# Performance work log

Hardware: AMD Instinct MI355X
Metric: run time of the kernel (lower is better)

## Reference

```python
import jax, jax.numpy as jnp
import numpy as np

BATCH = 4
N1 = 131072   # stage-1 voxels (total over batch)
N2 = 32768    # stage-2 (stride-2 downsampled) voxels
D_MODEL = 128
D_INNER = 2 * D_MODEL
D_STATE = 16
D_CONV = 4
DT_RANK = 8   # ceil(d_model / 16)
EPS = 1e-5


def _ln(x, g, b):
    mu = x.mean(-1, keepdims=True)
    v = ((x - mu) ** 2).mean(-1, keepdims=True)
    return (x - mu) * jax.lax.rsqrt(v + EPS) * g + b


def _causal_conv(x, w, b):
    # x: [B,L,Di], w: [Di,K] -> depthwise causal conv1d
    y = jax.lax.conv_general_dilated(
        x.transpose(0, 2, 1), w[:, None, :], (1,), [(D_CONV - 1, 0)],
        dimension_numbers=('NCH', 'OIH', 'NCH'), feature_group_count=D_INNER)
    return y.transpose(0, 2, 1) + b


def _mamba_block(x, ln_g, ln_b, in_w, conv_w, conv_b, xproj_w, dtproj_w, dtproj_b, A_log, Dp, out_w):
    # create_block: LayerNorm -> Mamba mixer (selective scan); returns hidden states
    h = _ln(x, ln_g, ln_b)
    xz = h @ in_w.T                          # [B,L,2*Di]
    xc, z = jnp.split(xz, 2, axis=-1)
    xc = jax.nn.silu(_causal_conv(xc, conv_w, conv_b))
    dbl = xc @ xproj_w.T                     # [B,L,dt_rank+2*d_state]
    dt = jax.nn.softplus(dbl[..., :DT_RANK] @ dtproj_w.T + dtproj_b)  # [B,L,Di]
    Bm = dbl[..., DT_RANK:DT_RANK + D_STATE]
    Cm = dbl[..., DT_RANK + D_STATE:]
    A = -jnp.exp(A_log)                      # [Di,ds]

    def step(hst, inp):
        dt_t, b_t, c_t, u_t = inp            # [B,Di],[B,ds],[B,ds],[B,Di]
        hst = jnp.exp(dt_t[..., None] * A) * hst + (dt_t * u_t)[..., None] * b_t[:, None, :]
        return hst, jnp.einsum('bds,bs->bd', hst, c_t)

    h0 = jnp.zeros((x.shape[0], D_INNER, D_STATE), x.dtype)
    xs = (dt.transpose(1, 0, 2), Bm.transpose(1, 0, 2), Cm.transpose(1, 0, 2), xc.transpose(1, 0, 2))
    _, ys = jax.lax.scan(step, h0, xs)       # ys: [L,B,Di]
    y = ys.transpose(1, 0, 2) + xc * Dp
    y = y * jax.nn.silu(z)
    return y @ out_w.T


def _mamba_params(key):
    ks = jax.random.split(key, 6)
    s = lambda k, sh, sc: jax.random.normal(k, sh, jnp.float32) * sc
    return dict(
        ln_g=jnp.ones((D_MODEL,), jnp.float32), ln_b=jnp.zeros((D_MODEL,), jnp.float32),
        in_w=s(ks[0], (2 * D_INNER, D_MODEL), 0.05),
        conv_w=s(ks[1], (D_INNER, D_CONV), 0.2), conv_b=jnp.zeros((D_INNER,), jnp.float32),
        xproj_w=s(ks[2], (DT_RANK + 2 * D_STATE, D_INNER), 0.05),
        dtproj_w=s(ks[3], (D_INNER, DT_RANK), 0.1), dtproj_b=s(ks[4], (D_INNER,), 0.1),
        A_log=jnp.log(jnp.tile(jnp.arange(1, D_STATE + 1, dtype=jnp.float32), (D_INNER, 1))),
        D=jnp.ones((D_INNER,), jnp.float32),
        out_w=s(ks[5], (D_MODEL, D_INNER), 0.05))


def setup_inputs():
    key = jax.random.key(0)
    k = jax.random.split(key, 10)
    inp = {
        'feats_s1': jax.random.normal(k[0], (N1, D_MODEL), jnp.float32),
        'feats_s2': jax.random.normal(k[1], (N2, D_MODEL), jnp.float32),
        'pos_s1': jax.random.uniform(k[2], (N1, 3), jnp.float32),
        'pos_s2': jax.random.uniform(k[3], (N2, 3), jnp.float32),
        'hilbert_s1': jax.random.randint(k[4], (N1,), 0, 1 << 30, jnp.int32),
        'hilbert_s2': jax.random.randint(k[5], (N2,), 0, 1 << 30, jnp.int32),
        'pe_w': jax.random.normal(k[6], (D_MODEL, 3), jnp.float32) * 0.1,
        'pe_b': jnp.zeros((D_MODEL,), jnp.float32),
        'norm_g': jnp.ones((D_MODEL,), jnp.float32), 'norm_b': jnp.zeros((D_MODEL,), jnp.float32),
        'normb_g': jnp.ones((D_MODEL,), jnp.float32), 'normb_b': jnp.zeros((D_MODEL,), jnp.float32),
    }
    for pref, kk in (('m1_', k[7]), ('m2_', k[8])):
        for n, v in _mamba_params(kk).items():
            inp[pref + n] = v
    return inp


def _forward(feats_s1, feats_s2, pos_s1, pos_s2, pe_w, pe_b, norm_g, norm_b, normb_g, normb_b,
             m1_ln_g, m1_ln_b, m1_in_w, m1_conv_w, m1_conv_b, m1_xproj_w, m1_dtproj_w, m1_dtproj_b, m1_A_log, m1_D, m1_out_w,
             m2_ln_g, m2_ln_b, m2_in_w, m2_conv_w, m2_conv_b, m2_xproj_w, m2_dtproj_w, m2_dtproj_b, m2_A_log, m2_D, m2_out_w,
             hilbert_s1, hilbert_s2):
    L1, L2 = N1 // BATCH, N2 // BATCH
    m1 = (m1_ln_g, m1_ln_b, m1_in_w, m1_conv_w, m1_conv_b, m1_xproj_w, m1_dtproj_w, m1_dtproj_b, m1_A_log, m1_D, m1_out_w)
    m2 = (m2_ln_g, m2_ln_b, m2_in_w, m2_conv_w, m2_conv_b, m2_xproj_w, m2_dtproj_w, m2_dtproj_b, m2_A_log, m2_D, m2_out_w)

    # stage 2: hilbert-order forward scan through mamba_layer1
    f2 = (feats_s2 + pos_s2 @ pe_w.T + pe_b).reshape(BATCH, L2, D_MODEL)
    o2 = jnp.argsort(hilbert_s2.reshape(BATCH, L2), axis=-1)          # inds_curt_to_next
    seq2 = jnp.take_along_axis(f2, o2[..., None], axis=1)
    out2 = _mamba_block(seq2, *m1)
    back2 = jnp.take_along_axis(out2, jnp.argsort(o2, axis=-1)[..., None], axis=1).reshape(N2, D_MODEL)
    out_s2 = _ln(back2, norm_g, norm_b)

    # stage 1: flipped hilbert-order (backward) scan through mamba_layer2
    f1 = (feats_s1 + pos_s1 @ pe_w.T + pe_b).reshape(BATCH, L1, D_MODEL)
    o1 = jnp.argsort(hilbert_s1.reshape(BATCH, L1), axis=-1)
    seq1 = jnp.take_along_axis(f1, o1[..., None], axis=1)[:, ::-1, :]
    out1 = _mamba_block(seq1, *m2)[:, ::-1, :]
    back1 = jnp.take_along_axis(out1, jnp.argsort(o1, axis=-1)[..., None], axis=1).reshape(N1, D_MODEL)
    out_s1 = _ln(back1, normb_g, normb_b)

    return jnp.concatenate([out_s1, out_s2], axis=0)   # [N1+N2, d_model]


def reference(feats_s1, feats_s2, pos_s1, pos_s2, pe_w, pe_b, norm_g, norm_b, normb_g, normb_b,
              m1_ln_g, m1_ln_b, m1_in_w, m1_conv_w, m1_conv_b, m1_xproj_w, m1_dtproj_w, m1_dtproj_b, m1_A_log, m1_D, m1_out_w,
              m2_ln_g, m2_ln_b, m2_in_w, m2_conv_w, m2_conv_b, m2_xproj_w, m2_dtproj_w, m2_dtproj_b, m2_A_log, m2_D, m2_out_w,
              hilbert_s1, hilbert_s2):
    return _forward(feats_s1, feats_s2, pos_s1, pos_s2, pe_w, pe_b, norm_g, norm_b, normb_g, normb_b,
                    m1_ln_g, m1_ln_b, m1_in_w, m1_conv_w, m1_conv_b, m1_xproj_w, m1_dtproj_w, m1_dtproj_b, m1_A_log, m1_D, m1_out_w,
                    m2_ln_g, m2_ln_b, m2_in_w, m2_conv_w, m2_conv_b, m2_xproj_w, m2_dtproj_w, m2_dtproj_b, m2_A_log, m2_D, m2_out_w,
                    hilbert_s1, hilbert_s2)
```

## Files before the change

### kernel.cpp

```cpp
#include <hip/hip_runtime.h>
#include <hip/hip_bf16.h>

#define DEV __device__ __forceinline__

constexpr int BATCH_ = 4;
constexpr int N1_ = 131072;
constexpr int N2_ = 32768;
constexpr int L1_ = N1_ / BATCH_;
constexpr int L2_ = N2_ / BATCH_;
constexpr int DM_ = 128;
constexpr int DI_ = 256;
constexpr int DS_ = 16;
constexpr int DTR_ = 8;
constexpr int TOT_ = N1_ + N2_;

constexpr int TA_ = 32;
constexpr int TAH_ = TA_ + 3;
constexpr int NTILE1_ = L1_ / TA_;
constexpr int NTILE2_ = L2_ / TA_;
constexpr int NTILES_ = 4 * NTILE1_ + 4 * NTILE2_;

constexpr int TS_ = 128;
constexpr int NCH1_ = L1_ / TS_;
constexpr int NCH2_ = L2_ / TS_;
constexpr int NCHUNKS_ = 4 * NCH1_ + 4 * NCH2_;

constexpr int NST_ = 160;

constexpr int IN1_OFF = 0;
constexpr int IN2_OFF = 65536;
constexpr int XP1_OFF = 131072;
constexpr int XP2_OFF = 143360;
constexpr int OW1_OFF = 155648;
constexpr int OW2_OFF = 188416;
constexpr int W16_TOT = 221184;

typedef short short8 __attribute__((ext_vector_type(8)));
typedef float f32x4 __attribute__((ext_vector_type(4)));

struct MP {
  const float* ln_g; const float* ln_b; const float* in_w;
  const float* conv_w; const float* conv_b; const float* xproj_w;
  const float* dtproj_w; const float* dtproj_b; const float* A_log;
  const float* Dp; const float* out_w;
};

DEV float softplusf(float x) {
  return fmaxf(x, 0.f) + __logf(1.f + __expf(-fabsf(x)));
}

DEV unsigned short f2bf(float f) {
  unsigned u = __builtin_bit_cast(unsigned, f);
  u += 0x7fffu + ((u >> 16) & 1u);
  return (unsigned short)(u >> 16);
}
DEV float bf2f(unsigned short s) {
  unsigned u = ((unsigned)s) << 16;
  return __builtin_bit_cast(float, u);
}

DEV void sort_tile_info(int tile, int& seg, int& tis, int& slotbase) {
  if (tile < 128) { seg = tile >> 5; tis = tile & 31; slotbase = seg * L1_; }
  else { seg = 4 + ((tile - 128) >> 3); tis = (tile - 128) & 7; slotbase = N1_ + (seg - 4) * L2_; }
}

__global__ __launch_bounds__(256) void k_prep(
    const float* __restrict__ in_w1, const float* __restrict__ xp1,
    const float* __restrict__ ow1,
    const float* __restrict__ in_w2, const float* __restrict__ xp2,
    const float* __restrict__ ow2,
    unsigned short* __restrict__ w16)
{
  const int i = blockIdx.x * 256 + threadIdx.x;
  if (i >= W16_TOT) return;
  float v;
  if (i < IN2_OFF) v = in_w1[i - IN1_OFF];
  else if (i < XP1_OFF) v = in_w2[i - IN2_OFF];
  else if (i < XP2_OFF) {
    const int j = i - XP1_OFF; const int r = j >> 8;
    v = (r < 40) ? xp1[j] : 0.f;
  } else if (i < OW1_OFF) {
    const int j = i - XP2_OFF; const int r = j >> 8;
    v = (r < 40) ? xp2[j] : 0.f;
  } else if (i < OW2_OFF) v = ow1[i - OW1_OFF];
  else v = ow2[i - OW2_OFF];
  w16[i] = f2bf(v);
}

__global__ __launch_bounds__(256) void k_hist(
    const int* __restrict__ hil1, const int* __restrict__ hil2,
    const unsigned* __restrict__ ksrc, unsigned* __restrict__ histg,
    int shift, int pass0)
{
  const int tile = blockIdx.x;
  int seg, tis, slotbase;
  sort_tile_info(tile, seg, tis, slotbase);
  const int tid = threadIdx.x;
  __shared__ unsigned h[1024];
  #pragma unroll
  for (int i = 0; i < 4; ++i) h[i * 256 + tid] = 0;
  __syncthreads();
  #pragma unroll
  for (int it = 0; it < 4; ++it) {
    const int li = tis * 1024 + it * 256 + tid;
    unsigned k;
    if (pass0) k = (unsigned)(seg < 4 ? hil1[seg * L1_ + li] : hil2[(seg - 4) * L2_ + li]);
    else       k = ksrc[slotbase + li];
    atomicAdd(&h[(k >> shift) & 1023u], 1u);
  }
  __syncthreads();
  #pragma unroll
  for (int i = 0; i < 4; ++i)
    histg[tile * 1024 + i * 256 + tid] = h[i * 256 + tid];
}

__global__ __launch_bounds__(256) void k_scanoff(
    const unsigned* __restrict__ histg, unsigned* __restrict__ offg)
{
  const int seg = blockIdx.x;
  const int ntiles = seg < 4 ? 32 : 8;
  const int tilebase = seg < 4 ? seg * 32 : 128 + (seg - 4) * 8;
  const int tid = threadIdx.x;
  const int d0 = tid * 4;
  unsigned tot[4] = {0, 0, 0, 0};
  for (int t = 0; t < ntiles; ++t) {
    const unsigned* hp = &histg[(size_t)(tilebase + t) * 1024 + d0];
    tot[0] += hp[0]; tot[1] += hp[1]; tot[2] += hp[2]; tot[3] += hp[3];
  }
  unsigned lp[4]; unsigned s = 0;
  #pragma unroll
  for (int j = 0; j < 4; ++j) { lp[j] = s; s += tot[j]; }
  const int lane = tid & 63, wv = tid >> 6;
  unsigned inc = s;
  #pragma unroll
  for (int off = 1; off < 64; off <<= 1) {
    unsigned v = (unsigned)__shfl_up((int)inc, off, 64);
    if (lane >= off) inc += v;
  }
  __shared__ unsigned wsum[4];
  if (lane == 63) wsum[wv] = inc;
  __syncthreads();
  unsigned wbase = 0;
  for (int w = 0; w < 4; ++w) if (w < wv) wbase += wsum[w];
  const unsigned base = wbase + inc - s;
  #pragma unroll
  for (int j = 0; j < 4; ++j) {
    unsigned run = base + lp[j];
    for (int t = 0; t < ntiles; ++t) {
      offg[(size_t)(tilebase + t) * 1024 + d0 + j] = run;
      run += histg[(size_t)(tilebase + t) * 1024 + d0 + j];
    }
  }
}

__global__ __launch_bounds__(256) void k_scatter(
    const int* __restrict__ hil1, const int* __restrict__ hil2,
    const unsigned* __restrict__ ksrc, const int* __restrict__ isrc,
    const unsigned* __restrict__ offg,
    unsigned* __restrict__ kdst, int* __restrict__ idst,
    int* __restrict__ o_all, int shift, int pass0, int last)
{
  const int tile = blockIdx.x;
  int seg, tis, slotbase;
  sort_tile_info(tile, seg, tis, slotbase);
  const int tid = threadIdx.x;
  const int lane = tid & 63, wv = tid >> 6;
  __shared__ unsigned runb[1024];
  __shared__ unsigned wcnt[4 * 1024];
  #pragma unroll
  for (int i = 0; i < 4; ++i) runb[i * 256 + tid] = offg[(size_t)tile * 1024 + i * 256 + tid];
  #pragma unroll
  for (int it = 0; it < 4; ++it) {
    #pragma unroll
    for (int i = 0; i < 16; ++i) wcnt[i * 256 + tid] = 0;
    __syncthreads();
    const int li = tis * 1024 + it * 256 + tid;
    unsigned k; int v;
    if (pass0) {
      k = (unsigned)(seg < 4 ? hil1[seg * L1_ + li] : hil2[(seg - 4) * L2_ + li]);
      v = li;
    } else {
      k = ksrc[slotbase + li]; v = isrc[slotbase + li];
    }
    const unsigned d = (k >> shift) & 1023u;
    unsigned long long m = ~0ull;
    #pragma unroll
    for (int b = 0; b < 10; ++b) {
      const unsigned long long bb = __ballot((int)((d >> b) & 1u));
      m &= ((d >> b) & 1u) ? bb : ~bb;
    }
    const unsigned lrank = (unsigned)__popcll(m & ((1ull << lane) - 1ull));
    wcnt[wv * 1024 + d] = (unsigned)__popcll(m);
    __syncthreads();
    unsigned prior = runb[d];
    for (int w = 0; w < 3; ++w) if (w < wv) prior += wcnt[w * 1024 + d];
    const unsigned pos = prior + lrank;
    if (last) o_all[slotbase + pos] = v;
    else { kdst[slotbase + pos] = k; idst[slotbase + pos] = v; }
    __syncthreads();
    #pragma unroll
    for (int i = 0; i < 4; ++i) {
      const int dd = i * 256 + tid;
      runb[dd] += wcnt[dd] + wcnt[1024 + dd] + wcnt[2048 + dd] + wcnt[3072 + dd];
    }
    __syncthreads();
  }
}

constexpr int HB_ = 136;
constexpr int XB_ = 264;
constexpr int OFF_HB16 = TAH_ * XB_ * 2;
constexpr int SMEM_A = OFF_HB16 + 48 * HB_ * 2;

__global__ __launch_bounds__(256) void k_phaseA(
    const float* __restrict__ feats1, const float* __restrict__ feats2,
    const float* __restrict__ pos1, const float* __restrict__ pos2,
    const float* __restrict__ pe_w, const float* __restrict__ pe_b,
    MP p1, MP p2, const int* __restrict__ o_all,
    const unsigned short* __restrict__ w16,
    __hip_bfloat16* __restrict__ xc_g, __hip_bfloat16* __restrict__ z_g,
    float* __restrict__ dbl_g)
{
  const int blk = blockIdx.x;
  bool is1; int b, tile;
  if (blk < 4 * NTILE1_) { is1 = true; b = blk / NTILE1_; tile = blk % NTILE1_; }
  else { const int r = blk - 4 * NTILE1_; is1 = false; b = r / NTILE2_; tile = r % NTILE2_; }
  const int L = is1 ? L1_ : L2_;
  const int slotbase = is1 ? b * L1_ : N1_ + b * L2_;
  const float* feats = is1 ? feats1 + (size_t)b * L1_ * DM_ : feats2 + (size_t)b * L2_ * DM_;
  const float* pos = is1 ? pos1 + (size_t)b * L1_ * 3 : pos2 + (size_t)b * L2_ * 3;
  const MP P = is1 ? p2 : p1;
  const unsigned short* iw16 = w16 + (is1 ? IN2_OFF : IN1_OFF);
  const unsigned short* xp16 = w16 + (is1 ? XP2_OFF : XP1_OFF);
  const bool rev = is1;
  const int t0 = tile * TA_;
  const int pstart = rev ? t0 : t0 - 3;
  const int lsh = rev ? 0 : 3;

  __shared__ char smem[SMEM_A];
  unsigned short* xcb16 = (unsigned short*)smem;
  unsigned short* hb16 = (unsigned short*)(smem + OFF_HB16);
  unsigned short* xc16 = xcb16;

  const int tid = threadIdx.x;
  const int lane = tid & 63, wv = tid >> 6;
  const int l15 = lane & 15, quad = lane >> 4;

  {
    unsigned* hz = (unsigned*)hb16;
    for (int i = tid; i < 13 * (HB_ / 2); i += 256)
      hz[TAH_ * (HB_ / 2) + i] = 0;
    const float pw00 = pe_w[lane * 3 + 0], pw01 = pe_w[lane * 3 + 1], pw02 = pe_w[lane * 3 + 2];
    const float pw10 = pe_w[(lane + 64) * 3 + 0], pw11 = pe_w[(lane + 64) * 3 + 1],
                pw12 = pe_w[(lane + 64) * 3 + 2];
    const float pb0 = pe_b[lane], pb1 = pe_b[lane + 64];
    const float g0 = P.ln_g[lane], g1 = P.ln_g[lane + 64];
    const float bt0 = P.ln_b[lane], bt1 = P.ln_b[lane + 64];
    #pragma unroll
    for (int k = 0; k < 9; ++k) {
      const int lt = wv + k * 4;
      if (lt >= TAH_) break;
      const int p = pstart + lt;
      unsigned short o0 = 0, o1 = 0;
      if (p >= 0 && p < L) {
        const int orig = o_all[slotbase + p];
        const float* fr = feats + (size_t)orig * DM_;
        const float* pr = pos + (size_t)orig * 3;
        const float c0 = pr[0], c1 = pr[1], c2 = pr[2];
        float x0 = fr[lane]      + c0 * pw00 + c1 * pw01 + c2 * pw02 + pb0;
        float x1 = fr[lane + 64] + c0 * pw10 + c1 * pw11 + c2 * pw12 + pb1;
        float s = x0 + x1, q = x0 * x0 + x1 * x1;
        #pragma unroll
        for (int off = 32; off; off >>= 1) {
          s += __shfl_xor(s, off, 64);
          q += __shfl_xor(q, off, 64);
        }
        const float mu = s * (1.f / 128.f);
        const float rs = rsqrtf(q * (1.f / 128.f) - mu * mu + 1e-5f);
        o0 = f2bf((x0 - mu) * rs * g0 + bt0);
        o1 = f2bf((x1 - mu) * rs * g1 + bt1);
      }
      hb16[lt * HB_ + lane]      = o0;
      hb16[lt * HB_ + lane + 64] = o1;
    }
  }
  __syncthreads();
  {
    short8 afr[3][4];
    #pragma unroll
    for (int mt = 0; mt < 3; ++mt)
      #pragma unroll
      for (int t = 0; t < 4; ++t)
        afr[mt][t] = *(const short8*)(hb16 + (mt * 16 + l15) * HB_ + t * 32 + quad * 8);
    for (int nn = 0; nn < 8; ++nn) {
      const int ntile = nn * 4 + wv;
      f32x4 acc[3];
      #pragma unroll
      for (int mt = 0; mt < 3; ++mt) acc[mt] = (f32x4){0.f, 0.f, 0.f, 0.f};
      #pragma unroll
      for (int t = 0; t < 4; ++t) {
        const short8 bfr = *(const short8*)(iw16 + (size_t)(ntile * 16 + l15) * DM_ + t * 32 + quad * 8);
        #pragma unroll
        for (int mt = 0; mt < 3; ++mt)
          acc[mt] = __builtin_amdgcn_mfma_f32_16x16x32_bf16(afr[mt][t], bfr, acc[mt], 0, 0, 0);
      }
      const int col = ntile * 16 + l15;
      if (col < 256) {
        #pragma unroll
        for (int mt = 0; mt < 3; ++mt)
          #pragma unroll
          for (int r = 0; r < 4; ++r) {
            const int row = mt * 16 + quad * 4 + r;
            if (row < TAH_) xcb16[row * XB_ + col] = f2bf(acc[mt][r]);
          }
      } else {
        #pragma unroll
        for (int mt = 0; mt < 3; ++mt)
          #pragma unroll
          for (int r = 0; r < 4; ++r) {
            const int row = mt * 16 + quad * 4 + r;
            const int m = row - lsh;
            if (m >= 0 && m < TA_)
              z_g[(size_t)(slotbase + t0 + m) * DI_ + (col - 256)] = __float2bfloat16(acc[mt][r]);
          }
      }
    }
  }
  __syncthreads();
  {
    const int d = tid;
    const float w0 = P.conv_w[d * 4 + 0], w1 = P.conv_w[d * 4 + 1],
                w2 = P.conv_w[d * 4 + 2], w3 = P.conv_w[d * 4 + 3];
    const float cb = P.conv_b[d];
    float x0 = bf2f(xcb16[0 * XB_ + d]), x1 = bf2f(xcb16[1 * XB_ + d]),
          x2 = bf2f(xcb16[2 * XB_ + d]);
    #pragma unroll
    for (int m = 0; m < TA_; ++m) {
      const float x3 = bf2f(xcb16[(m + 3) * XB_ + d]);
      float v;
      if (rev) v = w3 * x0 + w2 * x1 + w1 * x2 + w0 * x3;
      else     v = w0 * x0 + w1 * x1 + w2 * x2 + w3 * x3;
      v += cb;
      v = v * (1.f / (1.f + __expf(-v)));
      const unsigned short vb = f2bf(v);
      xc_g[(size_t)(slotbase + t0 + m) * DI_ + d] = __builtin_bit_cast(__hip_bfloat16, vb);
      xcb16[m * XB_ + d] = vb;
      x0 = x1; x1 = x2; x2 = x3;
    }
  }
  __syncthreads();
  if (wv < 3) {
    f32x4 acc0 = (f32x4){0.f,0.f,0.f,0.f}, acc1 = acc0;
    #pragma unroll
    for (int t = 0; t < 8; ++t) {
      const short8 bfr = *(const short8*)(xp16 + (size_t)(wv * 16 + l15) * DI_ + t * 32 + quad * 8);
      const short8 a0 = *(const short8*)(xc16 + (l15) * XB_ + t * 32 + quad * 8);
      const short8 a1 = *(const short8*)(xc16 + (16 + l15) * XB_ + t * 32 + quad * 8);
      acc0 = __builtin_amdgcn_mfma_f32_16x16x32_bf16(a0, bfr, acc0, 0, 0, 0);
      acc1 = __builtin_amdgcn_mfma_f32_16x16x32_bf16(a1, bfr, acc1, 0, 0, 0);
    }
    const int col = wv * 16 + l15;
    if (col < 40) {
      #pragma unroll
      for (int r = 0; r < 4; ++r) {
        dbl_g[(size_t)(slotbase + t0 + quad * 4 + r) * 40 + col] = acc0[r];
        dbl_g[(size_t)(slotbase + t0 + 16 + quad * 4 + r) * 40 + col] = acc1[r];
      }
    }
  }
}

struct ScanP {
  float Av[DS_]; float A0; bool fast;
  float dtw[DTR_]; float dtb;
};
DEV void load_scanp(const MP& P, int d, ScanP& sp) {
  #pragma unroll
  for (int s = 0; s < DS_; ++s) sp.Av[s] = -__expf(P.A_log[d * DS_ + s]);
  sp.A0 = sp.Av[0];
  bool f = true;
  #pragma unroll
  for (int s = 0; s < DS_; ++s)
    f = f && (fabsf(sp.Av[s] - (float)(s + 1) * sp.A0) <= 1e-3f * (float)(s + 1));
  sp.fast = f;
  #pragma unroll
  for (int r = 0; r < DTR_; ++r) sp.dtw[r] = P.dtproj_w[d * DTR_ + r];
  sp.dtb = P.dtproj_b[d];
}
DEV float dt_from(const float4& q0, const float4& q1, const ScanP& sp) {
  const float dtraw = sp.dtb
      + q0.x*sp.dtw[0] + q0.y*sp.dtw[1] + q0.z*sp.dtw[2] + q0.w*sp.dtw[3]
      + q1.x*sp.dtw[4] + q1.y*sp.dtw[5] + q1.z*sp.dtw[6] + q1.w*sp.dtw[7];
  return softplusf(dtraw);
}

__global__ __launch_bounds__(256) void k_scan1(
    MP p1, MP p2,
    const __hip_bfloat16* __restrict__ xc_g, const float* __restrict__ dbl_g,
    float* __restrict__ hloc, float* __restrict__ sumdt_g)
{
  const int blk = blockIdx.x;
  bool is1; int b, pc;
  if (blk < 4 * NCH1_) { is1 = true; b = blk / NCH1_; pc = blk % NCH1_; }
  else { const int r = blk - 4 * NCH1_; is1 = false; b = r / NCH2_; pc = r % NCH2_; }
  const MP P = is1 ? p2 : p1;
  const int L = is1 ? L1_ : L2_;
  const bool rev = is1;
  const int slotbase = is1 ? b * L1_ : N1_ + b * L2_;
  const int d = threadIdx.x;
  ScanP sp; load_scanp(P, d, sp);
  const unsigned short* xcp = (const unsigned short*)xc_g;
  float h[DS_];
  #pragma unroll
  for (int s = 0; s < DS_; ++s) h[s] = 0.f;
  float sdt = 0.f;
  const int s0 = rev ? (L - (pc + 1) * TS_) : pc * TS_;
  const int dp = rev ? -1 : 1;
  int slot = slotbase + (rev ? (s0 + TS_ - 1) : s0);
  if (sp.fast) {
    const float* dr = dbl_g + (size_t)slot * 40;
    float4 q0 = *(const float4*)dr, q1 = *(const float4*)(dr + 4);
    float4 Bv[4];
    #pragma unroll
    for (int j = 0; j < 4; ++j) Bv[j] = *(const float4*)(dr + 8 + 4 * j);
    float u = bf2f(xcp[(size_t)slot * DI_ + d]);
    for (int i = 0; i < TS_; ++i) {
      const int nslot = (i + 1 < TS_) ? slot + dp : slot;
      const float* nr = dbl_g + (size_t)nslot * 40;
      float4 nq0 = *(const float4*)nr, nq1 = *(const float4*)(nr + 4);
      float4 nB[4];
      #pragma unroll
      for (int j = 0; j < 4; ++j) nB[j] = *(const float4*)(nr + 8 + 4 * j);
      const float nu = bf2f(xcp[(size_t)nslot * DI_ + d]);
      const float dt = dt_from(q0, q1, sp);
      const float du = dt * u;
      sdt += dt;
      const float e1 = __expf(dt * sp.A0);
      const float e2 = e1 * e1, e3 = e2 * e1, e4 = e2 * e2;
      float base = 1.f;
      #pragma unroll
      for (int j = 0; j < 4; ++j) {
        const float m1 = base * e1, m2 = base * e2, m3 = base * e3, m4 = base * e4;
        h[4*j+0] = m1 * h[4*j+0] + du * Bv[j].x;
        h[4*j+1] = m2 * h[4*j+1] + du * Bv[j].y;
        h[4*j+2] = m3 * h[4*j+2] + du * Bv[j].z;
        h[4*j+3] = m4 * h[4*j+3] + du * Bv[j].w;
        base = m4;
      }
      slot = nslot; q0 = nq0; q1 = nq1; u = nu;
      #pragma unroll
      for (int j = 0; j < 4; ++j) Bv[j] = nB[j];
    }
  } else {
    for (int i = 0; i < TS_; ++i) {
      const float* dr = dbl_g + (size_t)slot * 40;
      const float4 q0 = *(const float4*)dr, q1 = *(const float4*)(dr + 4);
      const float dt = dt_from(q0, q1, sp);
      const float u = bf2f(xcp[(size_t)slot * DI_ + d]);
      const float du = dt * u;
      sdt += dt;
      float Bvv[16];
      #pragma unroll
      for (int j = 0; j < 4; ++j) *(float4*)&Bvv[4*j] = *(const float4*)(dr + 8 + 4*j);
      #pragma unroll
      for (int s = 0; s < DS_; ++s)
        h[s] = __expf(dt * sp.Av[s]) * h[s] + du * Bvv[s];
      slot += dp;
    }
  }
  float* hl = hloc + (size_t)blk * DS_ * DI_;
  #pragma unroll
  for (int s = 0; s < DS_; ++s) hl[s * DI_ + d] = h[s];
  sumdt_g[(size_t)blk * DI_ + d] = sdt;
}

__global__ __launch_bounds__(256) void k_scan2(
    MP p1, MP p2, const float* __restrict__ hloc,
    const float* __restrict__ sumdt_g, float* __restrict__ hin)
{
  const int seq = blockIdx.x >> 4;
  const int s = blockIdx.x & 15;
  const bool is1 = seq < 4;
  const int b = is1 ? seq : seq - 4;
  const MP P = is1 ? p2 : p1;
  const int nch = is1 ? NCH1_ : NCH2_;
  const int chbase = is1 ? b * NCH1_ : 4 * NCH1_ + b * NCH2_;
  const int d = threadIdx.x;
  const float A = -__expf(P.A_log[d * DS_ + s]);
  float carry = 0.f;
  for (int pc = 0; pc < nch; ++pc) {
    const size_t idx = (size_t)(chbase + pc);
    const float sdt = sumdt_g[idx * DI_ + d];
    hin[idx * DS_ * DI_ + s * DI_ + d] = carry;
    carry = __expf(A * sdt) * carry + hloc[idx * DS_ * DI_ + s * DI_ + d];
  }
}

__global__ __launch_bounds__(256) void k_scan3(
    MP p1, MP p2,
    const __hip_bfloat16* __restrict__ xc_g, const float* __restrict__ dbl_g,
    const float* __restrict__ hin, __hip_bfloat16* zv_g)
{
  const int blk = blockIdx.x;
  bool is1; int b, pc;
  if (blk < 4 * NCH1_) { is1 = true; b = blk / NCH1_; pc = blk % NCH1_; }
  else { const int r = blk - 4 * NCH1_; is1 = false; b = r / NCH2_; pc = r % NCH2_; }
  const MP P = is1 ? p2 : p1;
  const int L = is1 ? L1_ : L2_;
  const bool rev = is1;
  const int slotbase = is1 ? b * L1_ : N1_ + b * L2_;
  const int d = threadIdx.x;
  ScanP sp; load_scanp(P, d, sp);
  const float Dp = P.Dp[d];
  const unsigned short* xcp = (const unsigned short*)xc_g;
  unsigned short* zvp = (unsigned short*)zv_g;
  float h[DS_];
  const float* hi = hin + (size_t)blk * DS_ * DI_;
  #pragma unroll
  for (int s = 0; s < DS_; ++s) h[s] = hi[s * DI_ + d];
  const int s0 = rev ? (L - (pc + 1) * TS_) : pc * TS_;
  const int dp = rev ? -1 : 1;
  int slot = slotbase + (rev ? (s0 + TS_ - 1) : s0);
  if (sp.fast) {
    const float* dr = dbl_g + (size_t)slot * 40;
    float4 q0 = *(const float4*)dr, q1 = *(const float4*)(dr + 4);
    float4 Bv[4], Cv[4];
    #pragma unroll
    for (int j = 0; j < 4; ++j) {
      Bv[j] = *(const float4*)(dr + 8 + 4 * j);
      Cv[j] = *(const float4*)(dr + 24 + 4 * j);
    }
    float u = bf2f(xcp[(size_t)slot * DI_ + d]);
    float zv = bf2f(zvp[(size_t)slot * DI_ + d]);
    for (int i = 0; i < TS_; ++i) {
      const int nslot = (i + 1 < TS_) ? slot + dp : slot;
      const float* nr = dbl_g + (size_t)nslot * 40;
      float4 nq0 = *(const float4*)nr, nq1 = *(const float4*)(nr + 4);
      float4 nB[4], nC[4];
      #pragma unroll
      for (int j = 0; j < 4; ++j) {
        nB[j] = *(const float4*)(nr + 8 + 4 * j);
        nC[j] = *(const float4*)(nr + 24 + 4 * j);
      }
      const float nu = bf2f(xcp[(size_t)nslot * DI_ + d]);
      const float nz = bf2f(zvp[(size_t)nslot * DI_ + d]);
      const float dt = dt_from(q0, q1, sp);
      const float du = dt * u;
      const float e1 = __expf(dt * sp.A0);
      const float e2 = e1 * e1, e3 = e2 * e1, e4 = e2 * e2;
      float base = 1.f;
      float y = 0.f;
      #pragma unroll
      for (int j = 0; j < 4; ++j) {
        const float m1 = base * e1, m2 = base * e2, m3 = base * e3, m4 = base * e4;
        h[4*j+0] = m1 * h[4*j+0] + du * Bv[j].x;  y += h[4*j+0] * Cv[j].x;
        h[4*j+1] = m2 * h[4*j+1] + du * Bv[j].y;  y += h[4*j+1] * Cv[j].y;
        h[4*j+2] = m3 * h[4*j+2] + du * Bv[j].z;  y += h[4*j+2] * Cv[j].z;
        h[4*j+3] = m4 * h[4*j+3] + du * Bv[j].w;  y += h[4*j+3] * Cv[j].w;
        base = m4;
      }
      const float sg = zv / (1.f + __expf(-zv));
      zvp[(size_t)slot * DI_ + d] = f2bf((y + u * Dp) * sg);
      slot = nslot; q0 = nq0; q1 = nq1; u = nu; zv = nz;
      #pragma unroll
      for (int j = 0; j < 4; ++j) { Bv[j] = nB[j]; Cv[j] = nC[j]; }
    }
  } else {
    for (int i = 0; i < TS_; ++i) {
      const float* dr = dbl_g + (size_t)slot * 40;
      const float4 q0 = *(const float4*)dr, q1 = *(const float4*)(dr + 4);
      const float dt = dt_from(q0, q1, sp);
      const float u = bf2f(xcp[(size_t)slot * DI_ + d]);
      const float zv = bf2f(zvp[(size_t)slot * DI_ + d]);
      const float du = dt * u;
      float Bvv[16], Cvv[16];
      #pragma unroll
      for (int j = 0; j < 4; ++j) {
        *(float4*)&Bvv[4*j] = *(const float4*)(dr + 8 + 4*j);
        *(float4*)&Cvv[4*j] = *(const float4*)(dr + 24 + 4*j);
      }
      float y = 0.f;
      #pragma unroll
      for (int s = 0; s < DS_; ++s) {
        h[s] = __expf(dt * sp.Av[s]) * h[s] + du * Bvv[s];
        y += h[s] * Cvv[s];
      }
      const float sg = zv / (1.f + __expf(-zv));
      zvp[(size_t)slot * DI_ + d] = f2bf((y + u * Dp) * sg);
      slot += dp;
    }
  }
}

constexpr int OB_ = 132;
__global__ __launch_bounds__(256) void k_final(
    const __hip_bfloat16* __restrict__ v_g, const int* __restrict__ o_all,
    const unsigned short* __restrict__ w16,
    const float* __restrict__ norm_g, const float* __restrict__ norm_b,
    const float* __restrict__ normb_g, const float* __restrict__ normb_b,
    float* __restrict__ out)
{
  const int blk = blockIdx.x;
  bool is1; int b, tile;
  if (blk < 4 * NTILE1_) { is1 = true; b = blk / NTILE1_; tile = blk % NTILE1_; }
  else { const int r = blk - 4 * NTILE1_; is1 = false; b = r / NTILE2_; tile = r % NTILE2_; }
  const unsigned short* W = w16 + (is1 ? OW2_OFF : OW1_OFF);
  const float* gg = is1 ? normb_g : norm_g;
  const float* gb = is1 ? normb_b : norm_b;
  const int slotbase = is1 ? b * L1_ : N1_ + b * L2_;
  const int t0 = tile * TA_;
  __shared__ float obuf[TA_ * OB_];
  const int tid = threadIdx.x;
  const int lane = tid & 63, wv = tid >> 6;
  const int l15 = lane & 15, quad = lane >> 4;
  {
    const unsigned short* vp = (const unsigned short*)v_g + (size_t)(slotbase + t0) * DI_;
    f32x4 acc00 = (f32x4){0.f,0.f,0.f,0.f}, acc01 = acc00, acc10 = acc00, acc11 = acc00;
    #pragma unroll
    for (int t = 0; t < 8; ++t) {
      const short8 a0 = *(const short8*)(vp + (size_t)(l15) * DI_ + t * 32 + quad * 8);
      const short8 a1 = *(const short8*)(vp + (size_t)(16 + l15) * DI_ + t * 32 + quad * 8);
      const short8 b0 = *(const short8*)(W + (size_t)((wv) * 16 + l15) * DI_ + t * 32 + quad * 8);
      const short8 b1 = *(const short8*)(W + (size_t)((wv + 4) * 16 + l15) * DI_ + t * 32 + quad * 8);
      acc00 = __builtin_amdgcn_mfma_f32_16x16x32_bf16(a0, b0, acc00, 0, 0, 0);
      acc01 = __builtin_amdgcn_mfma_f32_16x16x32_bf16(a1, b0, acc01, 0, 0, 0);
      acc10 = __builtin_amdgcn_mfma_f32_16x16x32_bf16(a0, b1, acc10, 0, 0, 0);
      acc11 = __builtin_amdgcn_mfma_f32_16x16x32_bf16(a1, b1, acc11, 0, 0, 0);
    }
    const int col0 = wv * 16 + l15;
    const int col1 = (wv + 4) * 16 + l15;
    #pragma unroll
    for (int r = 0; r < 4; ++r) {
      obuf[(quad * 4 + r) * OB_ + col0] = acc00[r];
      obuf[(16 + quad * 4 + r) * OB_ + col0] = acc01[r];
      obuf[(quad * 4 + r) * OB_ + col1] = acc10[r];
      obuf[(16 + quad * 4 + r) * OB_ + col1] = acc11[r];
    }
  }
  __syncthreads();
  {
    for (int m = wv; m < TA_; m += 4) {
      float x0 = obuf[m * OB_ + lane], x1 = obuf[m * OB_ + lane + 64];
      float s = x0 + x1, q = x0 * x0 + x1 * x1;
      #pragma unroll
      for (int off = 32; off; off >>= 1) {
        s += __shfl_xor(s, off, 64);
        q += __shfl_xor(q, off, 64);
      }
      const float mu = s * (1.f / 128.f);
      const float rs = rsqrtf(q * (1.f / 128.f) - mu * mu + 1e-5f);
      const int orig = o_all[slotbase + t0 + m];
      float* orow = out + (size_t)(slotbase + orig) * DM_;
      orow[lane]      = (x0 - mu) * rs * gg[lane]      + gb[lane];
      orow[lane + 64] = (x1 - mu) * rs * gg[lane + 64] + gb[lane + 64];
    }
  }
}

extern "C" void kernel_launch(void* const* d_in, const int* in_sizes, int n_in,
                              void* d_out, int out_size, void* d_ws, size_t ws_size,
                              hipStream_t stream)
{
  (void)in_sizes; (void)n_in; (void)out_size; (void)ws_size;
  const float* feats1 = (const float*)d_in[0];
  const float* feats2 = (const float*)d_in[1];
  const float* pos1   = (const float*)d_in[2];
  const float* pos2   = (const float*)d_in[3];
  const int*   hil1   = (const int*)d_in[4];
  const int*   hil2   = (const int*)d_in[5];
  const float* pe_w   = (const float*)d_in[6];
  const float* pe_b   = (const float*)d_in[7];
  const float* norm_g  = (const float*)d_in[8];
  const float* norm_b  = (const float*)d_in[9];
  const float* normb_g = (const float*)d_in[10];
  const float* normb_b = (const float*)d_in[11];
  MP p1 { (const float*)d_in[12], (const float*)d_in[13], (const float*)d_in[14],
          (const float*)d_in[15], (const float*)d_in[16], (const float*)d_in[17],
          (const float*)d_in[18], (const float*)d_in[19], (const float*)d_in[20],
          (const float*)d_in[21], (const float*)d_in[22] };
  MP p2 { (const float*)d_in[23], (const float*)d_in[24], (const float*)d_in[25],
          (const float*)d_in[26], (const float*)d_in[27], (const float*)d_in[28],
          (const float*)d_in[29], (const float*)d_in[30], (const float*)d_in[31],
          (const float*)d_in[32], (const float*)d_in[33] };

  char* w = (char*)d_ws;
  auto take = [&](size_t bytes) -> char* {
    char* p = w; w += (bytes + 255) & ~(size_t)255; return p;
  };
  int* o_all = (int*)take((size_t)TOT_ * 4);
  unsigned* kA = (unsigned*)take((size_t)TOT_ * 4);
  int* iA = (int*)take((size_t)TOT_ * 4);
  unsigned* kB = (unsigned*)take((size_t)TOT_ * 4);
  int* iB = (int*)take((size_t)TOT_ * 4);
  unsigned* histg = (unsigned*)take((size_t)NST_ * 1024 * 4);
  unsigned* offg  = (unsigned*)take((size_t)NST_ * 1024 * 4);
  __hip_bfloat16* xc = (__hip_bfloat16*)take((size_t)TOT_ * DI_ * 2);
  __hip_bfloat16* vzb = (__hip_bfloat16*)take((size_t)TOT_ * DI_ * 2);
  float* dbl = (float*)take((size_t)TOT_ * 40 * 4);
  float* hloc = (float*)take((size_t)NCHUNKS_ * DS_ * DI_ * 4);
  float* hin  = (float*)take((size_t)NCHUNKS_ * DS_ * DI_ * 4);
  float* sdt  = (float*)take((size_t)NCHUNKS_ * DI_ * 4);
  unsigned short* w16 = (unsigned short*)take((size_t)W16_TOT * 2);

  hipLaunchKernelGGL(k_prep, dim3((W16_TOT + 255) / 256), dim3(256), 0, stream,
                     p1.in_w, p1.xproj_w, p1.out_w, p2.in_w, p2.xproj_w, p2.out_w, w16);
  hipLaunchKernelGGL(k_hist, dim3(NST_), dim3(256), 0, stream,
                     hil1, hil2, kB, histg, 0, 1);
  hipLaunchKernelGGL(k_scanoff, dim3(8), dim3(256), 0, stream, histg, offg);
  hipLaunchKernelGGL(k_scatter, dim3(NST_), dim3(256), 0, stream,
                     hil1, hil2, kB, iB, offg, kB, iB, o_all, 0, 1, 0);
  hipLaunchKernelGGL(k_hist, dim3(NST_), dim3(256), 0, stream,
                     hil1, hil2, kB, histg, 10, 0);
  hipLaunchKernelGGL(k_scanoff, dim3(8), dim3(256), 0, stream, histg, offg);
  hipLaunchKernelGGL(k_scatter, dim3(NST_), dim3(256), 0, stream,
                     hil1, hil2, kB, iB, offg, kA, iA, o_all, 10, 0, 0);
  hipLaunchKernelGGL(k_hist, dim3(NST_), dim3(256), 0, stream,
                     hil1, hil2, kA, histg, 20, 0);
  hipLaunchKernelGGL(k_scanoff, dim3(8), dim3(256), 0, stream, histg, offg);
  hipLaunchKernelGGL(k_scatter, dim3(NST_), dim3(256), 0, stream,
                     hil1, hil2, kA, iA, offg, kB, iB, o_all, 20, 0, 1);

  hipLaunchKernelGGL(k_phaseA, dim3(NTILES_), dim3(256), 0, stream,
                     feats1, feats2, pos1, pos2, pe_w, pe_b, p1, p2, o_all, w16,
                     xc, vzb, dbl);
  hipLaunchKernelGGL(k_scan1, dim3(NCHUNKS_), dim3(256), 0, stream,
                     p1, p2, xc, dbl, hloc, sdt);
  hipLaunchKernelGGL(k_scan2, dim3(128), dim3(256), 0, stream,
                     p1, p2, hloc, sdt, hin);
  hipLaunchKernelGGL(k_scan3, dim3(NCHUNKS_), dim3(256), 0, stream,
                     p1, p2, xc, dbl, hin, vzb);
  hipLaunchKernelGGL(k_final, dim3(NTILES_), dim3(256), 0, stream,
                     vzb, o_all, w16, norm_g, norm_b, normb_g, normb_b,
                     (float*)d_out);
}
```

Measured before the change: 887.6 us.

## Split gather+posenc+LayerNorm into separate kernel writing padded bf16 sequence

Moves the per-voxel gather, positional-encoding add and LayerNorm out of phaseA into a new k_gather kernel. That kernel writes a padded bf16 sequence buffer, so the 3-row conv halo is no longer recomputed per tile. phaseA now loads MFMA A-fragments straight from global memory instead of going through shared memory. This removes one __syncthreads and the redundant halo work, and restructures the MFMA loop to process two N-tiles per A-fragment set. The cost is an extra kernel launch plus a global write and read of the normalized sequence.

```diff
diff --git a/kernel.cpp b/kernel.cpp
--- a/kernel.cpp
+++ b/kernel.cpp
@@ -26,6 +26,11 @@
 constexpr int NCHUNKS_ = 4 * NCH1_ + 4 * NCH2_;
 
 constexpr int NST_ = 160;
+
+constexpr int PADR_ = 16;
+constexpr int SR1_ = L1_ + 2 * PADR_;
+constexpr int SR2_ = L2_ + 2 * PADR_;
+constexpr int RTOT_ = 4 * SR1_ + 4 * SR2_;
 
 constexpr int IN1_OFF = 0;
 constexpr int IN2_OFF = 65536;
@@ -207,16 +212,58 @@
   }
 }
 
-constexpr int HB_ = 136;
-constexpr int XB_ = 264;
-constexpr int OFF_HB16 = TAH_ * XB_ * 2;
-constexpr int SMEM_A = OFF_HB16 + 48 * HB_ * 2;
-
-__global__ __launch_bounds__(256) void k_phaseA(
+__global__ __launch_bounds__(256) void k_gather(
     const float* __restrict__ feats1, const float* __restrict__ feats2,
     const float* __restrict__ pos1, const float* __restrict__ pos2,
     const float* __restrict__ pe_w, const float* __restrict__ pe_b,
     MP p1, MP p2, const int* __restrict__ o_all,
+    unsigned* __restrict__ seq_g)
+{
+  const int wv = threadIdx.x >> 6, lane = threadIdx.x & 63;
+  const int prow = blockIdx.x * 4 + wv;
+  if (prow >= RTOT_) return;
+  int seg, within;
+  if (prow < 4 * SR1_) { seg = prow / SR1_; within = prow - seg * SR1_; }
+  else { const int r = prow - 4 * SR1_; seg = 4 + r / SR2_; within = r - (seg - 4) * SR2_; }
+  const bool is1 = seg < 4;
+  const int b = is1 ? seg : seg - 4;
+  const int L = is1 ? L1_ : L2_;
+  const int p = within - PADR_;
+  unsigned outw = 0;
+  if (p >= 0 && p < L) {
+    const int slotbase = is1 ? b * L1_ : N1_ + b * L2_;
+    const int orig = o_all[slotbase + p];
+    const MP P = is1 ? p2 : p1;
+    const float* fr = (is1 ? feats1 + (size_t)b * L1_ * DM_
+                           : feats2 + (size_t)b * L2_ * DM_) + (size_t)orig * DM_;
+    const float* pr = (is1 ? pos1 + (size_t)b * L1_ * 3
+                           : pos2 + (size_t)b * L2_ * 3) + (size_t)orig * 3;
+    const int c0 = 2 * lane;
+    const float2 f = *(const float2*)(fr + c0);
+    const float q0 = pr[0], q1 = pr[1], q2 = pr[2];
+    float x0 = f.x + q0 * pe_w[c0 * 3 + 0] + q1 * pe_w[c0 * 3 + 1] + q2 * pe_w[c0 * 3 + 2] + pe_b[c0];
+    float x1 = f.y + q0 * pe_w[c0 * 3 + 3] + q1 * pe_w[c0 * 3 + 4] + q2 * pe_w[c0 * 3 + 5] + pe_b[c0 + 1];
+    float s = x0 + x1, qq = x0 * x0 + x1 * x1;
+    #pragma unroll
+    for (int off = 32; off; off >>= 1) {
+      s += __shfl_xor(s, off, 64);
+      qq += __shfl_xor(qq, off, 64);
+    }
+    const float mu = s * (1.f / 128.f);
+    const float rs = rsqrtf(qq * (1.f / 128.f) - mu * mu + 1e-5f);
+    const unsigned short o0 = f2bf((x0 - mu) * rs * P.ln_g[c0]     + P.ln_b[c0]);
+    const unsigned short o1 = f2bf((x1 - mu) * rs * P.ln_g[c0 + 1] + P.ln_b[c0 + 1]);
+    outw = (unsigned)o0 | ((unsigned)o1 << 16);
+  }
+  seq_g[(size_t)prow * 64 + lane] = outw;
+}
+
+constexpr int XB_ = 264;
+constexpr int SMEM_A = TAH_ * XB_ * 2;
+
+__global__ __launch_bounds__(256) void k_phaseA(
+    MP p1, MP p2,
+    const unsigned short* __restrict__ seq_g,
     const unsigned short* __restrict__ w16,
     __hip_bfloat16* __restrict__ xc_g, __hip_bfloat16* __restrict__ z_g,
     float* __restrict__ dbl_g)
@@ -225,13 +272,12 @@
   bool is1; int b, tile;
   if (blk < 4 * NTILE1_) { is1 = true; b = blk / NTILE1_; tile = blk % NTILE1_; }
   else { const int r = blk - 4 * NTILE1_; is1 = false; b = r / NTILE2_; tile = r % NTILE2_; }
-  const int L = is1 ? L1_ : L2_;
   const int slotbase = is1 ? b * L1_ : N1_ + b * L2_;
-  const float* feats = is1 ? feats1 + (size_t)b * L1_ * DM_ : feats2 + (size_t)b * L2_ * DM_;
-  const float* pos = is1 ? pos1 + (size_t)b * L1_ * 3 : pos2 + (size_t)b * L2_ * 3;
   const MP P = is1 ? p2 : p1;
   const unsigned short* iw16 = w16 + (is1 ? IN2_OFF : IN1_OFF);
   const unsigned short* xp16 = w16 + (is1 ? XP2_OFF : XP1_OFF);
+  const int segrow0 = is1 ? b * SR1_ : 4 * SR1_ + b * SR2_;
+  const unsigned short* seq = seq_g + (size_t)segrow0 * DM_;
   const bool rev = is1;
   const int t0 = tile * TA_;
   const int pstart = rev ? t0 : t0 - 3;
@@ -239,90 +285,51 @@
 
   __shared__ char smem[SMEM_A];
   unsigned short* xcb16 = (unsigned short*)smem;
-  unsigned short* hb16 = (unsigned short*)(smem + OFF_HB16);
   unsigned short* xc16 = xcb16;
 
   const int tid = threadIdx.x;
   const int lane = tid & 63, wv = tid >> 6;
   const int l15 = lane & 15, quad = lane >> 4;
 
-  {
-    unsigned* hz = (unsigned*)hb16;
-    for (int i = tid; i < 13 * (HB_ / 2); i += 256)
-      hz[TAH_ * (HB_ / 2) + i] = 0;
-    const float pw00 = pe_w[lane * 3 + 0], pw01 = pe_w[lane * 3 + 1], pw02 = pe_w[lane * 3 + 2];
-    const float pw10 = pe_w[(lane + 64) * 3 + 0], pw11 = pe_w[(lane + 64) * 3 + 1],
-                pw12 = pe_w[(lane + 64) * 3 + 2];
-    const float pb0 = pe_b[lane], pb1 = pe_b[lane + 64];
-    const float g0 = P.ln_g[lane], g1 = P.ln_g[lane + 64];
-    const float bt0 = P.ln_b[lane], bt1 = P.ln_b[lane + 64];
-    #pragma unroll
-    for (int k = 0; k < 9; ++k) {
-      const int lt = wv + k * 4;
-      if (lt >= TAH_) break;
-      const int p = pstart + lt;
-      unsigned short o0 = 0, o1 = 0;
-      if (p >= 0 && p < L) {
-        const int orig = o_all[slotbase + p];
-        const float* fr = feats + (size_t)orig * DM_;
-        const float* pr = pos + (size_t)orig * 3;
-        const float c0 = pr[0], c1 = pr[1], c2 = pr[2];
-        float x0 = fr[lane]      + c0 * pw00 + c1 * pw01 + c2 * pw02 + pb0;
-        float x1 = fr[lane + 64] + c0 * pw10 + c1 * pw11 + c2 * pw12 + pb1;
-        float s = x0 + x1, q = x0 * x0 + x1 * x1;
-        #pragma unroll
-        for (int off = 32; off; off >>= 1) {
-          s += __shfl_xor(s, off, 64);
-          q += __shfl_xor(q, off, 64);
+  #pragma unroll
+  for (int mt = 0; mt < 3; ++mt) {
+    const int arow = PADR_ + pstart + mt * 16 + l15;
+    short8 afr[4];
+    #pragma unroll
+    for (int t = 0; t < 4; ++t)
+      afr[t] = *(const short8*)(seq + (size_t)arow * DM_ + t * 32 + quad * 8);
+    #pragma unroll
+    for (int nn2 = 0; nn2 < 4; ++nn2) {
+      const int ntA = nn2 * 8 + wv;
+      const int ntB = nn2 * 8 + 4 + wv;
+      f32x4 accA = (f32x4){0.f, 0.f, 0.f, 0.f}, accB = accA;
+      #pragma unroll
+      for (int t = 0; t < 4; ++t) {
+        const short8 bfA = *(const short8*)(iw16 + (size_t)(ntA * 16 + l15) * DM_ + t * 32 + quad * 8);
+        const short8 bfB = *(const short8*)(iw16 + (size_t)(ntB * 16 + l15) * DM_ + t * 32 + quad * 8);
+        accA = __builtin_amdgcn_mfma_f32_16x16x32_bf16(afr[t], bfA, accA, 0, 0, 0);
+        accB = __builtin_amdgcn_mfma_f32_16x16x32_bf16(afr[t], bfB, accB, 0, 0, 0);
+      }
+      const int row0 = mt * 16 + quad * 4;
+      const int colA = ntA * 16 + l15;
+      const int colB = ntB * 16 + l15;
+      #pragma unroll
+      for (int r = 0; r < 4; ++r) {
+        const int row = row0 + r;
+        if (colA < 256) {
+          if (row < TAH_) xcb16[row * XB_ + colA] = f2bf(accA[r]);
+        } else {
+          const int m = row - lsh;
+          if (m >= 0 && m < TA_)
+            z_g[(size_t)(slotbase + t0 + m) * DI_ + (colA - 256)] = __float2bfloat16(accA[r]);
         }
-        const float mu = s * (1.f / 128.f);
-        const float rs = rsqrtf(q * (1.f / 128.f) - mu * mu + 1e-5f);
-        o0 = f2bf((x0 - mu) * rs * g0 + bt0);
-        o1 = f2bf((x1 - mu) * rs * g1 + bt1);
-      }
-      hb16[lt * HB_ + lane]      = o0;
-      hb16[lt * HB_ + lane + 64] = o1;
-    }
-  }
-  __syncthreads();
-  {
-    short8 afr[3][4];
-    #pragma unroll
-    for (int mt = 0; mt < 3; ++mt)
-      #pragma unroll
-      for (int t = 0; t < 4; ++t)
-        afr[mt][t] = *(const short8*)(hb16 + (mt * 16 + l15) * HB_ + t * 32 + quad * 8);
-    for (int nn = 0; nn < 8; ++nn) {
-      const int ntile = nn * 4 + wv;
-      f32x4 acc[3];
-      #pragma unroll
-      for (int mt = 0; mt < 3; ++mt) acc[mt] = (f32x4){0.f, 0.f, 0.f, 0.f};
-      #pragma unroll
-      for (int t = 0; t < 4; ++t) {
-        const short8 bfr = *(const short8*)(iw16 + (size_t)(ntile * 16 + l15) * DM_ + t * 32 + quad * 8);
-        #pragma unroll
-        for (int mt = 0; mt < 3; ++mt)
-          acc[mt] = __builtin_amdgcn_mfma_f32_16x16x32_bf16(afr[mt][t], bfr, acc[mt], 0, 0, 0);
-      }
-      const int col = ntile * 16 + l15;
-      if (col < 256) {
-        #pragma unroll
-        for (int mt = 0; mt < 3; ++mt)
-          #pragma unroll
-          for (int r = 0; r < 4; ++r) {
-            const int row = mt * 16 + quad * 4 + r;
-            if (row < TAH_) xcb16[row * XB_ + col] = f2bf(acc[mt][r]);
-          }
-      } else {
-        #pragma unroll
-        for (int mt = 0; mt < 3; ++mt)
-          #pragma unroll
-          for (int r = 0; r < 4; ++r) {
-            const int row = mt * 16 + quad * 4 + r;
-            const int m = row - lsh;
-            if (m >= 0 && m < TA_)
-              z_g[(size_t)(slotbase + t0 + m) * DI_ + (col - 256)] = __float2bfloat16(acc[mt][r]);
-          }
+        if (colB < 256) {
+          if (row < TAH_) xcb16[row * XB_ + colB] = f2bf(accB[r]);
+        } else {
+          const int m = row - lsh;
+          if (m >= 0 && m < TA_)
+            z_g[(size_t)(slotbase + t0 + m) * DI_ + (colB - 256)] = __float2bfloat16(accB[r]);
+        }
       }
     }
   }
@@ -701,6 +708,7 @@
   float* hin  = (float*)take((size_t)NCHUNKS_ * DS_ * DI_ * 4);
   float* sdt  = (float*)take((size_t)NCHUNKS_ * DI_ * 4);
   unsigned short* w16 = (unsigned short*)take((size_t)W16_TOT * 2);
+  unsigned* seq = (unsigned*)take((size_t)RTOT_ * DM_ * 2);
 
   hipLaunchKernelGGL(k_prep, dim3((W16_TOT + 255) / 256), dim3(256), 0, stream,
                      p1.in_w, p1.xproj_w, p1.out_w, p2.in_w, p2.xproj_w, p2.out_w, w16);
@@ -720,9 +728,10 @@
   hipLaunchKernelGGL(k_scatter, dim3(NST_), dim3(256), 0, stream,
                      hil1, hil2, kA, iA, offg, kB, iB, o_all, 20, 0, 1);
 
+  hipLaunchKernelGGL(k_gather, dim3((RTOT_ + 3) / 4), dim3(256), 0, stream,
+                     feats1, feats2, pos1, pos2, pe_w, pe_b, p1, p2, o_all, seq);
   hipLaunchKernelGGL(k_phaseA, dim3(NTILES_), dim3(256), 0, stream,
-                     feats1, feats2, pos1, pos2, pe_w, pe_b, p1, p2, o_all, w16,
-                     xc, vzb, dbl);
+                     p1, p2, (const unsigned short*)seq, w16, xc, vzb, dbl);
   hipLaunchKernelGGL(k_scan1, dim3(NCHUNKS_), dim3(256), 0, stream,
                      p1, p2, xc, dbl, hloc, sdt);
   hipLaunchKernelGGL(k_scan2, dim3(128), dim3(256), 0, stream,
```

Result: slower. 989.1 us (+11.4%).
